# Kernel optimization log

Measured on AMD Instinct MI355X. Metric: run time of the kernel, lower is better.

The kernel has to match this reference:

```python
import jax, jax.numpy as jnp
import numpy as np

# BEV plane bounds: matches IPM(xbound=[-50,50,0.5], ybound=[-50,50,0.5], z=0, angles=0)
XB = (-50.0, 50.0, 0.5)
YB = (-50.0, 50.0, 0.5)
BEV_W = int((XB[1] - XB[0]) / XB[2])  # 200
BEV_H = int((YB[1] - YB[0]) / YB[2])  # 200


def _plane_xyz():
    """Homogeneous world-plane grid [4, BEV_H*BEV_W] (rotation is identity since angles=0)."""
    x = np.linspace(XB[0], XB[1], BEV_W)
    y = np.linspace(YB[0], YB[1], BEV_H)
    xg, yg = np.meshgrid(x, y)  # (BEV_H, BEV_W)
    xf, yf = xg.flatten(), yg.flatten()
    z = np.zeros_like(xf)  # plane z = 0
    coords = np.stack([yf, xf, z, np.ones_like(xf)], axis=0)
    return jnp.asarray(coords, jnp.float32)


def _rotation_from_euler(roll, pitch, yaw):
    si, sj, sk = np.sin(np.deg2rad([roll, pitch, yaw]))
    ci, cj, ck = np.cos(np.deg2rad([roll, pitch, yaw]))
    cc, cs, sc, ss = ci * ck, ci * sk, si * ck, si * sk
    R = np.identity(4)
    R[0, 0] = cj * ck; R[0, 1] = sj * sc - cs; R[0, 2] = sj * cc + ss
    R[1, 0] = cj * sk; R[1, 1] = sj * ss + cc; R[1, 2] = sj * cs - sc
    R[2, 0] = -sj;     R[2, 1] = cj * si;      R[2, 2] = cj * ci
    return R


def setup_inputs() -> dict:
    key = jax.random.key(0)
    k1, k2, k3 = jax.random.split(key, 3)
    B, N, H, W, C = 2, 6, 128, 352, 32
    images = jax.random.normal(k1, (B, N, H, W, C), jnp.float32)
    # Structured intrinsics (focal 200, principal point at image center) + small noise
    K = np.eye(4); K[0, 0] = 200.0; K[1, 1] = 200.0; K[0, 2] = W / 2.0; K[1, 2] = H / 2.0
    Ks = np.tile(K[None], (B * N, 1, 1))
    yaws = [0.0, 60.0, 120.0, 180.0, 240.0, 300.0]
    RTs = np.zeros((B * N, 4, 4))
    for i in range(B * N):
        R = _rotation_from_euler(0.0, -90.0, yaws[i % N])  # camera looking down at plane
        R[2, 3] = 2.0  # camera height
        RTs[i] = R
    Ks = jnp.asarray(Ks, jnp.float32) + 0.01 * jax.random.normal(k2, (B * N, 4, 4), jnp.float32)
    RTs = jnp.asarray(RTs, jnp.float32) + 0.001 * jax.random.normal(k3, (B * N, 4, 4), jnp.float32)
    return {"images": images, "Ks": Ks, "RTs": RTs}


def _ipm_forward(images, Ks, RTs):
    B, N, H, W, C = images.shape
    BN = B * N
    imgs = images.reshape(BN, H, W, C)
    xyz = _plane_xyz()  # [4, h*w]
    h, w = BEV_H, BEV_W
    eps = 1e-7
    # Perspective projection: P @ xyz -> pixel coords [BN, h, w, 2]
    P = (Ks @ RTs).reshape(-1, 4, 4)
    pc = P @ xyz  # [BN, 4, h*w]
    pix = pc[:, :2, :] / (pc[:, 2:3, :] + eps)  # [BN, 2, h*w]
    pix = pix.reshape(BN, 2, h, w).transpose(0, 2, 3, 1)  # [BN, h, w, 2]
    # Bilinear sampling (clamp-to-border, matching the torch code ordering:
    # floor -> clip corners -> weights from CLIPPED corners)
    pix_x = pix[..., 0:1]
    pix_y = pix[..., 1:2]
    x0 = jnp.floor(pix_x); x1 = x0 + 1.0
    y0 = jnp.floor(pix_y); y1 = y0 + 1.0
    x_max, y_max = float(W - 1), float(H - 1)
    x0 = jnp.clip(x0, 0.0, x_max); x1 = jnp.clip(x1, 0.0, x_max)
    y0 = jnp.clip(y0, 0.0, y_max); y1 = jnp.clip(y1, 0.0, y_max)
    wt_x0 = x1 - pix_x; wt_x1 = pix_x - x0
    wt_y0 = y1 - pix_y; wt_y1 = pix_y - y0
    base_y0 = y0 * W; base_y1 = y1 * W
    imgs_flat = imgs.reshape(BN, H * W, C)
    def gather(flat_idx):  # flat_idx: [BN, h, w, 1] float -> gathered [BN, h, w, C]
        idx = flat_idx.reshape(BN, -1, 1).astype(jnp.int32)
        return jnp.take_along_axis(imgs_flat, idx, axis=1).reshape(BN, h, w, C)
    im00 = gather(x0 + base_y0)
    im01 = gather(x0 + base_y1)
    im10 = gather(x1 + base_y0)
    im11 = gather(x1 + base_y1)
    out = (wt_x0 * wt_y0) * im00 + (wt_x0 * wt_y1) * im01 \
        + (wt_x1 * wt_y0) * im10 + (wt_x1 * wt_y1) * im11
    out = out.reshape(B, N, h, w, C)
    return out.max(axis=1)  # [B, h, w, C]


def reference(images, Ks, RTs):
    return _ipm_forward(images, Ks, RTs)
```

## Files before the change

### kernel.cpp

```cpp
#include <hip/hip_runtime.h>
#include <math.h>

#define NUM_CAM   12
#define CAM_PER_B 6
#define IMG_H     128
#define IMG_W     352
#define CH        32
#define BEV       200
#define PIX_PER_B (BEV * BEV)
#define PIX_PER_BLOCK 32
#define BLOCKS_PER_B (PIX_PER_B / PIX_PER_BLOCK)

__global__ __launch_bounds__(256) void ipm_kernel(
    const float* __restrict__ imgs,
    const float* __restrict__ Ks,
    const float* __restrict__ RTs,
    float* __restrict__ out)
{
    __shared__ float sP[CAM_PER_B][9];

    const int tid = threadIdx.x;
    const int b = blockIdx.x / BLOCKS_PER_B;

    if (tid < CAM_PER_B * 9) {
        const int cl = tid / 9;
        const int k  = tid % 9;
        const int r  = k / 3;
        const int cc = k % 3;
        const int col = (cc == 2) ? 3 : cc;
        const float* K  = Ks  + (b * CAM_PER_B + cl) * 16;
        const float* RT = RTs + (b * CAM_PER_B + cl) * 16;
        float acc = 0.0f;
        #pragma unroll
        for (int kk = 0; kk < 4; ++kk)
            acc += K[r * 4 + kk] * RT[kk * 4 + col];
        sP[cl][k] = acc;
    }
    __syncthreads();

    const int px_in_block = tid >> 3;
    const int c4 = (tid & 7) * 4;
    const int pix_id = blockIdx.x * PIX_PER_BLOCK + px_in_block;
    const int rem = pix_id - b * PIX_PER_B;
    const int gy = rem / BEV;
    const int gx = rem - gy * BEV;

    const double step = 100.0 / 199.0;
    const float xf = (float)(-50.0 + (double)gx * step);
    const float yf = (float)(-50.0 + (double)gy * step);

    float4 best = make_float4(-INFINITY, -INFINITY, -INFINITY, -INFINITY);

    #pragma unroll
    for (int n = 0; n < CAM_PER_B; ++n) {
        const float p00 = sP[n][0], p01 = sP[n][1], p03 = sP[n][2];
        const float p10 = sP[n][3], p11 = sP[n][4], p13 = sP[n][5];
        const float p20 = sP[n][6], p21 = sP[n][7], p23 = sP[n][8];

        const float den = (p20 * yf + p21 * xf + p23) + 1e-7f;
        const float px  = (p00 * yf + p01 * xf + p03) / den;
        const float py  = (p10 * yf + p11 * xf + p13) / den;

        const float x0f = floorf(px);
        const float y0f = floorf(py);

        float4 val = make_float4(0.0f, 0.0f, 0.0f, 0.0f);
        if (x0f >= 0.0f && x0f <= (float)(IMG_W - 2) &&
            y0f >= 0.0f && y0f <= (float)(IMG_H - 2)) {
            const float wx1 = px - x0f;
            const float wx0 = (x0f + 1.0f) - px;
            const float wy1 = py - y0f;
            const float wy0 = (y0f + 1.0f) - py;

            const int xi = (int)x0f;
            const int yi = (int)y0f;
            const int cam = b * CAM_PER_B + n;
            const float* base =
                imgs + (((size_t)cam * IMG_H + yi) * IMG_W + xi) * CH + c4;

            const float4 a00 = *(const float4*)(base);
            const float4 a10 = *(const float4*)(base + CH);
            const float4 a01 = *(const float4*)(base + (size_t)IMG_W * CH);
            const float4 a11 = *(const float4*)(base + (size_t)IMG_W * CH + CH);

            const float w00 = wx0 * wy0;
            const float w01 = wx0 * wy1;
            const float w10 = wx1 * wy0;
            const float w11 = wx1 * wy1;

            val.x = ((w00 * a00.x + w01 * a01.x) + w10 * a10.x) + w11 * a11.x;
            val.y = ((w00 * a00.y + w01 * a01.y) + w10 * a10.y) + w11 * a11.y;
            val.z = ((w00 * a00.z + w01 * a01.z) + w10 * a10.z) + w11 * a11.z;
            val.w = ((w00 * a00.w + w01 * a01.w) + w10 * a10.w) + w11 * a11.w;
        }

        best.x = fmaxf(best.x, val.x);
        best.y = fmaxf(best.y, val.y);
        best.z = fmaxf(best.z, val.z);
        best.w = fmaxf(best.w, val.w);
    }

    *(float4*)(out + (size_t)pix_id * CH + c4) = best;
}

extern "C" void kernel_launch(void* const* d_in, const int* in_sizes, int n_in,
                              void* d_out, int out_size, void* d_ws, size_t ws_size,
                              hipStream_t stream) {
    const float* images = (const float*)d_in[0];
    const float* Ks     = (const float*)d_in[1];
    const float* RTs    = (const float*)d_in[2];
    float* out          = (float*)d_out;

    const int total_blocks = 2 * BLOCKS_PER_B;
    ipm_kernel<<<total_blocks, 256, 0, stream>>>(images, Ks, RTs, out);
}
```

Before: 100.4 us.

## Hoist all camera projections, issue gathers unconditionally with clamped addresses, nontemporal store

Splits the per-camera loop into two phases. The first computes projections, weights, validity flags and clamped base addresses for all six cameras; the second issues every bilinear gather without branching and zeroes invalid results with a select. This removes divergent branches and lets all 24 float4 loads be in flight at once to hide memory latency. The cost is extra register pressure and loads for out-of-range cameras that are later discarded. The output write now uses a nontemporal store to avoid polluting the cache.

```diff
diff --git a/kernel.cpp b/kernel.cpp
--- a/kernel.cpp
+++ b/kernel.cpp
@@ -10,6 +10,8 @@
 #define PIX_PER_B (BEV * BEV)
 #define PIX_PER_BLOCK 32
 #define BLOCKS_PER_B (PIX_PER_B / PIX_PER_BLOCK)
+
+typedef float vfloat4 __attribute__((ext_vector_type(4)));
 
 __global__ __launch_bounds__(256) void ipm_kernel(
     const float* __restrict__ imgs,
@@ -49,7 +51,9 @@
     const float xf = (float)(-50.0 + (double)gx * step);
     const float yf = (float)(-50.0 + (double)gy * step);
 
-    float4 best = make_float4(-INFINITY, -INFINITY, -INFINITY, -INFINITY);
+    const float* bases[CAM_PER_B];
+    float w00[CAM_PER_B], w01[CAM_PER_B], w10[CAM_PER_B], w11[CAM_PER_B];
+    bool  valid[CAM_PER_B];
 
     #pragma unroll
     for (int n = 0; n < CAM_PER_B; ++n) {
@@ -64,35 +68,49 @@
         const float x0f = floorf(px);
         const float y0f = floorf(py);
 
-        float4 val = make_float4(0.0f, 0.0f, 0.0f, 0.0f);
-        if (x0f >= 0.0f && x0f <= (float)(IMG_W - 2) &&
-            y0f >= 0.0f && y0f <= (float)(IMG_H - 2)) {
-            const float wx1 = px - x0f;
-            const float wx0 = (x0f + 1.0f) - px;
-            const float wy1 = py - y0f;
-            const float wy0 = (y0f + 1.0f) - py;
+        valid[n] = (x0f >= 0.0f) & (x0f <= (float)(IMG_W - 2)) &
+                   (y0f >= 0.0f) & (y0f <= (float)(IMG_H - 2));
 
-            const int xi = (int)x0f;
-            const int yi = (int)y0f;
-            const int cam = b * CAM_PER_B + n;
-            const float* base =
-                imgs + (((size_t)cam * IMG_H + yi) * IMG_W + xi) * CH + c4;
+        const float wx1 = px - x0f;
+        const float wx0 = (x0f + 1.0f) - px;
+        const float wy1 = py - y0f;
+        const float wy0 = (y0f + 1.0f) - py;
+        w00[n] = wx0 * wy0;
+        w01[n] = wx0 * wy1;
+        w10[n] = wx1 * wy0;
+        w11[n] = wx1 * wy1;
 
-            const float4 a00 = *(const float4*)(base);
-            const float4 a10 = *(const float4*)(base + CH);
-            const float4 a01 = *(const float4*)(base + (size_t)IMG_W * CH);
-            const float4 a11 = *(const float4*)(base + (size_t)IMG_W * CH + CH);
+        const float xc = fminf(fmaxf(x0f, 0.0f), (float)(IMG_W - 2));
+        const float yc = fminf(fmaxf(y0f, 0.0f), (float)(IMG_H - 2));
+        const int xi = (int)xc;
+        const int yi = (int)yc;
+        const int cam = b * CAM_PER_B + n;
+        bases[n] = imgs + (((size_t)cam * IMG_H + yi) * IMG_W + xi) * CH + c4;
+    }
 
-            const float w00 = wx0 * wy0;
-            const float w01 = wx0 * wy1;
-            const float w10 = wx1 * wy0;
-            const float w11 = wx1 * wy1;
+    float4 best = make_float4(-INFINITY, -INFINITY, -INFINITY, -INFINITY);
 
-            val.x = ((w00 * a00.x + w01 * a01.x) + w10 * a10.x) + w11 * a11.x;
-            val.y = ((w00 * a00.y + w01 * a01.y) + w10 * a10.y) + w11 * a11.y;
-            val.z = ((w00 * a00.z + w01 * a01.z) + w10 * a10.z) + w11 * a11.z;
-            val.w = ((w00 * a00.w + w01 * a01.w) + w10 * a10.w) + w11 * a11.w;
-        }
+    #pragma unroll
+    for (int n = 0; n < CAM_PER_B; ++n) {
+        const float* base = bases[n];
+        const float4 a00 = *(const float4*)(base);
+        const float4 a10 = *(const float4*)(base + CH);
+        const float4 a01 = *(const float4*)(base + (size_t)IMG_W * CH);
+        const float4 a11 = *(const float4*)(base + (size_t)IMG_W * CH + CH);
+
+        const float c00 = w00[n], c01 = w01[n];
+        const float c10 = w10[n], c11 = w11[n];
+
+        float4 val;
+        val.x = ((c00 * a00.x + c01 * a01.x) + c10 * a10.x) + c11 * a11.x;
+        val.y = ((c00 * a00.y + c01 * a01.y) + c10 * a10.y) + c11 * a11.y;
+        val.z = ((c00 * a00.z + c01 * a01.z) + c10 * a10.z) + c11 * a11.z;
+        val.w = ((c00 * a00.w + c01 * a01.w) + c10 * a10.w) + c11 * a11.w;
+
+        val.x = valid[n] ? val.x : 0.0f;
+        val.y = valid[n] ? val.y : 0.0f;
+        val.z = valid[n] ? val.z : 0.0f;
+        val.w = valid[n] ? val.w : 0.0f;
 
         best.x = fmaxf(best.x, val.x);
         best.y = fmaxf(best.y, val.y);
@@ -100,7 +118,9 @@
         best.w = fmaxf(best.w, val.w);
     }
 
-    *(float4*)(out + (size_t)pix_id * CH + c4) = best;
+    vfloat4 bv;
+    bv.x = best.x; bv.y = best.y; bv.z = best.z; bv.w = best.w;
+    __builtin_nontemporal_store(bv, (vfloat4*)(out + (size_t)pix_id * CH + c4));
 }
 
 extern "C" void kernel_launch(void* const* d_in, const int* in_sizes, int n_in,
```

Measured after the change: 103.7 us. +3.3%, slower.

## Precompute per-pixel projections in shared memory once per block and stream outputs

Applied to the files above, without the earlier changes.

Each block now computes the projection, bilinear weights and base offset for each of its 32 pixels and 6 cameras once, using 192 threads, and stores them in shared memory. This removes the redundant per-channel-thread division and floor work that eight threads per pixel used to repeat. The gather threads then only read offsets and weights. The output store becomes a nontemporal store, and launch bounds request 6 blocks per SIMD-level occupancy. The cost is an extra shared-memory round trip, plus each thread now recomputing K·RT instead of sharing it.

```diff
diff --git a/kernel.cpp b/kernel.cpp
--- a/kernel.cpp
+++ b/kernel.cpp
@@ -11,96 +11,119 @@
 #define PIX_PER_BLOCK 32
 #define BLOCKS_PER_B (PIX_PER_B / PIX_PER_BLOCK)
 
-__global__ __launch_bounds__(256) void ipm_kernel(
+typedef float vfloat4 __attribute__((ext_vector_type(4)));
+
+__global__ __launch_bounds__(256, 6) void ipm_kernel(
     const float* __restrict__ imgs,
     const float* __restrict__ Ks,
     const float* __restrict__ RTs,
     float* __restrict__ out)
 {
-    __shared__ float sP[CAM_PER_B][9];
+    __shared__ float sw00[CAM_PER_B][PIX_PER_BLOCK];
+    __shared__ float sw01[CAM_PER_B][PIX_PER_BLOCK];
+    __shared__ float sw10[CAM_PER_B][PIX_PER_BLOCK];
+    __shared__ float sw11[CAM_PER_B][PIX_PER_BLOCK];
+    __shared__ int   soff[CAM_PER_B][PIX_PER_BLOCK];
 
     const int tid = threadIdx.x;
     const int b = blockIdx.x / BLOCKS_PER_B;
 
-    if (tid < CAM_PER_B * 9) {
-        const int cl = tid / 9;
-        const int k  = tid % 9;
-        const int r  = k / 3;
-        const int cc = k % 3;
-        const int col = (cc == 2) ? 3 : cc;
-        const float* K  = Ks  + (b * CAM_PER_B + cl) * 16;
-        const float* RT = RTs + (b * CAM_PER_B + cl) * 16;
-        float acc = 0.0f;
+    if (tid < CAM_PER_B * PIX_PER_BLOCK) {
+        const int cam = tid >> 5;
+        const int pix = tid & 31;
+        const int pix_id = blockIdx.x * PIX_PER_BLOCK + pix;
+        const int rem = pix_id - b * PIX_PER_B;
+        const int gy = rem / BEV;
+        const int gx = rem - gy * BEV;
+
+        const double step = 100.0 / 199.0;
+        const float xf = (float)(-50.0 + (double)gx * step);
+        const float yf = (float)(-50.0 + (double)gy * step);
+
+        const int cg = b * CAM_PER_B + cam;
+        const float* K  = Ks  + cg * 16;
+        const float* RT = RTs + cg * 16;
+
+        float P[9];
         #pragma unroll
-        for (int kk = 0; kk < 4; ++kk)
-            acc += K[r * 4 + kk] * RT[kk * 4 + col];
-        sP[cl][k] = acc;
+        for (int r = 0; r < 3; ++r) {
+            #pragma unroll
+            for (int cc = 0; cc < 3; ++cc) {
+                const int col = (cc == 2) ? 3 : cc;
+                float acc = 0.0f;
+                #pragma unroll
+                for (int kk = 0; kk < 4; ++kk)
+                    acc += K[r * 4 + kk] * RT[kk * 4 + col];
+                P[r * 3 + cc] = acc;
+            }
+        }
+
+        const float den = (P[6] * yf + P[7] * xf + P[8]) + 1e-7f;
+        const float px  = (P[0] * yf + P[1] * xf + P[2]) / den;
+        const float py  = (P[3] * yf + P[4] * xf + P[5]) / den;
+
+        const float x0f = floorf(px);
+        const float y0f = floorf(py);
+
+        const bool valid = (x0f >= 0.0f) & (x0f <= (float)(IMG_W - 2)) &
+                           (y0f >= 0.0f) & (y0f <= (float)(IMG_H - 2));
+
+        sw10[cam][pix] = px - x0f;
+        sw00[cam][pix] = (x0f + 1.0f) - px;
+        sw11[cam][pix] = py - y0f;
+        sw01[cam][pix] = (y0f + 1.0f) - py;
+
+        int off = -1;
+        if (valid) {
+            const int xi = (int)x0f;
+            const int yi = (int)y0f;
+            off = ((cg * IMG_H + yi) * IMG_W + xi) * CH;
+        }
+        soff[cam][pix] = off;
     }
     __syncthreads();
 
-    const int px_in_block = tid >> 3;
-    const int c4 = (tid & 7) * 4;
-    const int pix_id = blockIdx.x * PIX_PER_BLOCK + px_in_block;
-    const int rem = pix_id - b * PIX_PER_B;
-    const int gy = rem / BEV;
-    const int gx = rem - gy * BEV;
-
-    const double step = 100.0 / 199.0;
-    const float xf = (float)(-50.0 + (double)gx * step);
-    const float yf = (float)(-50.0 + (double)gy * step);
+    const int pix = tid >> 3;
+    const int c4  = (tid & 7) * 4;
+    const int pix_id = blockIdx.x * PIX_PER_BLOCK + pix;
 
     float4 best = make_float4(-INFINITY, -INFINITY, -INFINITY, -INFINITY);
 
     #pragma unroll
     for (int n = 0; n < CAM_PER_B; ++n) {
-        const float p00 = sP[n][0], p01 = sP[n][1], p03 = sP[n][2];
-        const float p10 = sP[n][3], p11 = sP[n][4], p13 = sP[n][5];
-        const float p20 = sP[n][6], p21 = sP[n][7], p23 = sP[n][8];
+        const int off = soff[n][pix];
+        float4 val = make_float4(0.0f, 0.0f, 0.0f, 0.0f);
+        if (off >= 0) {
+            const float wx0 = sw00[n][pix];
+            const float wy0 = sw01[n][pix];
+            const float wx1 = sw10[n][pix];
+            const float wy1 = sw11[n][pix];
 
-        const float den = (p20 * yf + p21 * xf + p23) + 1e-7f;
-        const float px  = (p00 * yf + p01 * xf + p03) / den;
-        const float py  = (p10 * yf + p11 * xf + p13) / den;
-
-        const float x0f = floorf(px);
-        const float y0f = floorf(py);
-
-        float4 val = make_float4(0.0f, 0.0f, 0.0f, 0.0f);
-        if (x0f >= 0.0f && x0f <= (float)(IMG_W - 2) &&
-            y0f >= 0.0f && y0f <= (float)(IMG_H - 2)) {
-            const float wx1 = px - x0f;
-            const float wx0 = (x0f + 1.0f) - px;
-            const float wy1 = py - y0f;
-            const float wy0 = (y0f + 1.0f) - py;
-
-            const int xi = (int)x0f;
-            const int yi = (int)y0f;
-            const int cam = b * CAM_PER_B + n;
-            const float* base =
-                imgs + (((size_t)cam * IMG_H + yi) * IMG_W + xi) * CH + c4;
-
+            const float* base = imgs + off + c4;
             const float4 a00 = *(const float4*)(base);
             const float4 a10 = *(const float4*)(base + CH);
-            const float4 a01 = *(const float4*)(base + (size_t)IMG_W * CH);
-            const float4 a11 = *(const float4*)(base + (size_t)IMG_W * CH + CH);
+            const float4 a01 = *(const float4*)(base + IMG_W * CH);
+            const float4 a11 = *(const float4*)(base + IMG_W * CH + CH);
 
-            const float w00 = wx0 * wy0;
-            const float w01 = wx0 * wy1;
-            const float w10 = wx1 * wy0;
-            const float w11 = wx1 * wy1;
+            const float c00 = wx0 * wy0;
+            const float c01 = wx0 * wy1;
+            const float c10 = wx1 * wy0;
+            const float c11 = wx1 * wy1;
 
-            val.x = ((w00 * a00.x + w01 * a01.x) + w10 * a10.x) + w11 * a11.x;
-            val.y = ((w00 * a00.y + w01 * a01.y) + w10 * a10.y) + w11 * a11.y;
-            val.z = ((w00 * a00.z + w01 * a01.z) + w10 * a10.z) + w11 * a11.z;
-            val.w = ((w00 * a00.w + w01 * a01.w) + w10 * a10.w) + w11 * a11.w;
+            val.x = ((c00 * a00.x + c01 * a01.x) + c10 * a10.x) + c11 * a11.x;
+            val.y = ((c00 * a00.y + c01 * a01.y) + c10 * a10.y) + c11 * a11.y;
+            val.z = ((c00 * a00.z + c01 * a01.z) + c10 * a10.z) + c11 * a11.z;
+            val.w = ((c00 * a00.w + c01 * a01.w) + c10 * a10.w) + c11 * a11.w;
         }
-
         best.x = fmaxf(best.x, val.x);
         best.y = fmaxf(best.y, val.y);
         best.z = fmaxf(best.z, val.z);
         best.w = fmaxf(best.w, val.w);
     }
 
-    *(float4*)(out + (size_t)pix_id * CH + c4) = best;
+    vfloat4 bv;
+    bv.x = best.x; bv.y = best.y; bv.z = best.z; bv.w = best.w;
+    __builtin_nontemporal_store(bv, (vfloat4*)(out + (size_t)pix_id * CH + c4));
 }
 
 extern "C" void kernel_launch(void* const* d_in, const int* in_sizes, int n_in,
```

Result: no change. 99.56 us (-0.9%).
